# Performance work log

Measured on AMD Instinct MI355X. Metric: run time of the kernel, lower is better.

## Reference

```python
import jax, jax.numpy as jnp
import numpy as np

BEAM_SIZE = 16


def setup_inputs() -> dict:
    key = jax.random.key(0)
    ks = jax.random.split(key, 9)
    B, N, S, A, Ai, E = 4, 48, 32, 16, 8, 512
    unaries = jax.random.normal(ks[0], (B, N, S), jnp.float32)
    behaviors = jax.random.normal(ks[1], (B, N, S, A), jnp.float32)
    interactions = jax.random.normal(ks[2], (B, N, N, S, S, Ai), jnp.float32)
    masks = jnp.ones((B, N), jnp.bool_)
    behavior_masks = jax.random.bernoulli(ks[3], 0.5, (S, A))
    interaction_masks = jax.random.bernoulli(ks[4], 0.5, (S, S, Ai))
    binary_edges = jax.random.randint(ks[5], (B, E, 2), 0, N, jnp.int32)
    binary_masks = jnp.ones((B, E), jnp.bool_)
    targets = jax.random.randint(ks[6], (B, N), 0, S, jnp.int32)
    weight_param_unary = jax.random.uniform(ks[7], (S,), jnp.float32)
    weight_param_binary = jax.random.uniform(ks[8], (S, S), jnp.float32)
    return dict(unaries=unaries, behaviors=behaviors, interactions=interactions,
                weight_param_unary=weight_param_unary, weight_param_binary=weight_param_binary,
                masks=masks, behavior_masks=behavior_masks, interaction_masks=interaction_masks,
                binary_edges=binary_edges, binary_masks=binary_masks, targets=targets)


def _forward(unaries, behaviors, interactions, weight_param_unary, weight_param_binary,
             masks, behavior_masks, interaction_masks, binary_edges, binary_masks, targets):
    sg = jax.lax.stop_gradient  # mirrors torch.no_grad blocks
    B, N, S = unaries.shape
    E = binary_edges.shape[1]
    K = min(BEAM_SIZE, S)
    dt = unaries.dtype

    m = masks[..., None].astype(dt)                                  # (B,N,1)
    masked_unaries = sg(unaries * m)                                 # no_grad
    bmask = behavior_masks.astype(dt)                                # (S,A)
    acnt = bmask.sum(-1)
    acnt = jnp.where(acnt == 0, jnp.ones((), dt), acnt)              # (S,)
    behaviors_unaries = sg(((behaviors * bmask).sum(-1) / acnt) * m) # (B,N,S), no_grad

    weighted_unaries = masked_unaries + weight_param_unary * behaviors_unaries

    # --- beam selection (targets forced to beam slot 0 via +inf scatter) ---
    bi = jnp.arange(B)[:, None]
    ni = jnp.arange(N)[None, :]
    _u = weighted_unaries.at[bi, ni, targets].set(jnp.inf)
    beam_targets = jax.lax.top_k(sg(_u), K)[1]                       # (B,N,K) int
    beam_unary = jnp.take_along_axis(weighted_unaries, beam_targets, axis=2)  # (B,N,K)

    # --- binary potentials: masked mean over interaction actions ---
    imask = interaction_masks.astype(dt)                             # (S,S,Ai)
    icnt = imask.sum(-1)
    icnt = jnp.where(icnt == 0, jnp.ones((), dt), icnt)              # (S,S)
    masked_inter = (interactions * imask).sum(-1) / icnt             # (B,N,N,S,S)

    eb = jnp.arange(B)[:, None]
    sel = masked_inter[eb, binary_edges[..., 0], binary_edges[..., 1]]  # (B,E,S,S)
    bt1 = beam_targets[eb, binary_edges[..., 0]]                     # (B,E,K)
    bt2 = beam_targets[eb, binary_edges[..., 1]]                     # (B,E,K)
    bin_phis_init = sg(sel[jnp.arange(B)[:, None, None, None],
                           jnp.arange(E)[None, :, None, None],
                           bt1[:, :, :, None], bt2[:, :, None, :]])  # (B,E,K,K), no_grad
    bin_phis = bin_phis_init * weight_param_binary[bt1[:, :, :, None], bt2[:, :, None, :]]

    # --- piecewise pseudo-likelihood loss ---
    norm_unary = jax.nn.log_softmax(beam_unary, axis=-1)
    gold_unary = jnp.where(masks, norm_unary[:, :, 0], jnp.zeros((), dt))
    pll = gold_unary.sum(-1)                                         # (B,)
    norm_bin = jax.nn.log_softmax(bin_phis.reshape(B, E, K * K), axis=-1).reshape(B, E, K, K)
    gold_bin = jnp.where(binary_masks, norm_bin[:, :, 0, 0], jnp.zeros((), dt))
    pll = pll + gold_bin.sum(-1)
    nll = -(pll / masks.sum(-1).astype(dt)).mean()
    return nll


def reference(unaries, behaviors, interactions, weight_param_unary, weight_param_binary,
              masks, behavior_masks, interaction_masks, binary_edges, binary_masks, targets):
    return _forward(unaries, behaviors, interactions, weight_param_unary, weight_param_binary,
                    masks, behavior_masks, interaction_masks, binary_edges, binary_masks, targets)
```

## Files before the change

kernel.cpp:

```cpp
#include <hip/hip_runtime.h>
#include <hip/hip_bf16.h>
#include <math.h>

#define BB 4
#define NN 48
#define SS 32
#define AA 16
#define AI 8
#define EE 512
#define KK 16
#define NNODE (BB * NN)
#define NEDGE (BB * EE)

#define WS_CBIN  0
#define WS_BEAM  32768
#define WS_NG    45056
#define WS_EG    46080

__device__ __forceinline__ bool read_mask(const void* p, int idx, int flag) {
    if (flag == 1) return ((const unsigned char*)p)[idx] != 0;
    if (flag == 2) return ((const float*)p)[idx] != 0.0f;
    return ((const int*)p)[idx] != 0;
}

__device__ __forceinline__ int detect_flag(const void* bmask, int lane) {
    unsigned int wrd = ((const unsigned int*)bmask)[lane & 31];
    bool anyF = __any(wrd == 0x3F800000u);
    bool anyG = __any(wrd > 1u);
    return anyF ? 2 : (anyG ? 1 : 0);
}

__global__ __launch_bounds__(256) void node_kernel(
    const float* __restrict__ unaries,
    const float* __restrict__ behaviors,
    const float* __restrict__ wpu,
    const float* __restrict__ wpb,
    const void* masks, const void* bmask, const void* imask,
    const int* __restrict__ targets,
    float* __restrict__ cbin,
    int* __restrict__ beam,
    float* __restrict__ node_gold)
{
    int tid = threadIdx.x;
    int wid = tid >> 6, lane = tid & 63;
    int flag = detect_flag(bmask, lane);

    if (blockIdx.x < 48) {
        int node = blockIdx.x * 4 + wid;
        float m = read_mask(masks, node, flag) ? 1.f : 0.f;
        int tgt = targets[node];

        float val = -INFINITY, key = -INFINITY;
        if (lane < SS) {
            int s = lane;
            float u = unaries[node * SS + s];
            const float* bp = behaviors + ((size_t)node * SS + s) * AA;
            float cnt = 0.f, raw = 0.f;
            #pragma unroll
            for (int a = 0; a < AA; ++a) {
                bool mm = read_mask(bmask, s * AA + a, flag);
                cnt += mm ? 1.f : 0.f;
                raw += mm ? bp[a] : 0.f;
            }
            if (cnt == 0.f) cnt = 1.f;
            val = m * (u + wpu[s] * (raw / cnt));
            key = (s == tgt) ? INFINITY : val;
        }

        int rank = 0;
        #pragma unroll
        for (int t = 0; t < SS; ++t) {
            float kt = __shfl(key, t, 64);
            rank += (kt > key) || (kt == key && t < lane);
        }
        bool sel = (lane < SS) && (rank < KK);
        if (sel) beam[node * KK + rank] = lane;

        float mv = sel ? val : -INFINITY;
        #pragma unroll
        for (int off = 32; off >= 1; off >>= 1)
            mv = fmaxf(mv, __shfl_xor(mv, off, 64));
        float se = sel ? expf(val - mv) : 0.f;
        #pragma unroll
        for (int off = 32; off >= 1; off >>= 1)
            se += __shfl_xor(se, off, 64);
        float vt = __shfl(val, tgt, 64);
        if (lane == 0)
            node_gold[node] = (m > 0.f) ? (vt - mv - logf(se)) : 0.f;
    } else {
        int idx = (blockIdx.x - 48) * 256 + tid;
        int p = idx >> 3;
        float cnt = 0.f;
        #pragma unroll
        for (int a = 0; a < AI; ++a)
            cnt += read_mask(imask, p * AI + a, flag) ? 1.f : 0.f;
        if (cnt == 0.f) cnt = 1.f;
        bool mm = read_mask(imask, idx, flag);
        cbin[idx] = mm ? (wpb[p] / cnt) : 0.f;
    }
}

__global__ __launch_bounds__(256) void edge_kernel(
    const float* __restrict__ interactions,
    const int* __restrict__ edges,
    const void* binmask, const void* bmask,
    const float* __restrict__ cbin,
    const int* __restrict__ beam,
    float* __restrict__ edge_gold)
{
    int be = blockIdx.x;
    int b = be >> 9;
    int tid = threadIdx.x;
    int wid = tid >> 6, lane = tid & 63;

    int n1 = edges[be * 2 + 0];
    int n2 = edges[be * 2 + 1];

    int i = tid >> 4, j = tid & 15;
    int s1 = beam[(b * NN + n1) * KK + i];
    int s2 = beam[(b * NN + n2) * KK + j];
    int p = s1 * SS + s2;

    size_t base = (((size_t)(b * NN + n1) * NN + n2) * (SS * SS) + p) * AI;
    float4 x0 = *(const float4*)(interactions + base);
    float4 x1 = *(const float4*)(interactions + base + 4);
    float4 c0 = *(const float4*)(cbin + p * AI);
    float4 c1 = *(const float4*)(cbin + p * AI + 4);
    float phi = x0.x * c0.x + x0.y * c0.y + x0.z * c0.z + x0.w * c0.w
              + x1.x * c1.x + x1.y * c1.y + x1.z * c1.z + x1.w * c1.w;

    __shared__ float sred[4];
    float v = phi;
    #pragma unroll
    for (int off = 32; off >= 1; off >>= 1)
        v = fmaxf(v, __shfl_xor(v, off, 64));
    if (lane == 0) sred[wid] = v;
    __syncthreads();
    float mx = fmaxf(fmaxf(sred[0], sred[1]), fmaxf(sred[2], sred[3]));
    __syncthreads();
    float e = expf(phi - mx);
    #pragma unroll
    for (int off = 32; off >= 1; off >>= 1)
        e += __shfl_xor(e, off, 64);
    if (lane == 0) sred[wid] = e;
    __syncthreads();
    if (tid == 0) {
        int flag = detect_flag(bmask, lane);
        float s = sred[0] + sred[1] + sred[2] + sred[3];
        float gold = phi - mx - logf(s);
        bool bm = read_mask(binmask, be, flag);
        edge_gold[be] = bm ? gold : 0.f;
    }
}

__global__ __launch_bounds__(256) void final_kernel(
    const void* masks, const void* bmask,
    const float* __restrict__ node_gold,
    const float* __restrict__ edge_gold,
    float* __restrict__ out)
{
    int tid = threadIdx.x;
    int b = tid >> 6;
    int lane = tid & 63;
    int flag = detect_flag(bmask, lane);

    float sum = 0.f, cnt = 0.f;
    if (lane < NN) {
        sum += node_gold[b * NN + lane];
        cnt += read_mask(masks, b * NN + lane, flag) ? 1.f : 0.f;
    }
    for (int e = lane; e < EE; e += 64)
        sum += edge_gold[b * EE + e];

    #pragma unroll
    for (int off = 32; off >= 1; off >>= 1) {
        sum += __shfl_xor(sum, off, 64);
        cnt += __shfl_xor(cnt, off, 64);
    }
    __shared__ float sp[4];
    if (lane == 0) sp[b] = sum / cnt;
    __syncthreads();
    if (tid == 0)
        out[0] = -(sp[0] + sp[1] + sp[2] + sp[3]) * (1.f / BB);
}

extern "C" void kernel_launch(void* const* d_in, const int* in_sizes, int n_in,
                              void* d_out, int out_size, void* d_ws, size_t ws_size,
                              hipStream_t stream) {
    const float* unaries      = (const float*)d_in[0];
    const float* behaviors    = (const float*)d_in[1];
    const float* interactions = (const float*)d_in[2];
    const float* wpu          = (const float*)d_in[3];
    const float* wpb          = (const float*)d_in[4];
    const void*  masks        = d_in[5];
    const void*  bmask        = d_in[6];
    const void*  imask        = d_in[7];
    const int*   edges        = (const int*)d_in[8];
    const void*  binmask      = d_in[9];
    const int*   targets      = (const int*)d_in[10];
    float* out = (float*)d_out;

    char* ws = (char*)d_ws;
    float* cbin      = (float*)(ws + WS_CBIN);
    int*   beamp     = (int*)(ws + WS_BEAM);
    float* node_gold = (float*)(ws + WS_NG);
    float* edge_gold = (float*)(ws + WS_EG);

    node_kernel<<<80, 256, 0, stream>>>(unaries, behaviors, wpu, wpb,
                                        masks, bmask, imask, targets,
                                        cbin, beamp, node_gold);
    edge_kernel<<<NEDGE, 256, 0, stream>>>(interactions, edges, binmask, bmask,
                                           cbin, beamp, edge_gold);
    final_kernel<<<1, 256, 0, stream>>>(masks, bmask, node_gold, edge_gold, out);
}
```

Before: 21.64 us.

## Fuse node beam selection into edge kernel, recomputing beams per edge

Merges the node and edge kernels into a single launch. Each 64-thread edge block recomputes the beam for both endpoint nodes in its two half-waves, so the beam and the precomputed binary coefficients no longer pass through global workspace and one launch plus its dependency disappear. Each lane now handles four pairs and computes the masked interaction average inline, and the block-level reductions become single-wave shuffles with no LDS barriers. The cost is redundant unary and behavior recomputation for every edge, plus mask reads repeated per pair.

```diff
diff --git a/kernel.cpp b/kernel.cpp
--- a/kernel.cpp
+++ b/kernel.cpp
@@ -12,10 +12,8 @@
 #define NNODE (BB * NN)
 #define NEDGE (BB * EE)
 
-#define WS_CBIN  0
-#define WS_BEAM  32768
-#define WS_NG    45056
-#define WS_EG    46080
+#define WS_NG    0
+#define WS_EG    1024
 
 __device__ __forceinline__ bool read_mask(const void* p, int idx, int flag) {
     if (flag == 1) return ((const unsigned char*)p)[idx] != 0;
@@ -30,126 +28,133 @@
     return anyF ? 2 : (anyG ? 1 : 0);
 }
 
-__global__ __launch_bounds__(256) void node_kernel(
+__device__ __forceinline__ void node_vals(
+    int node, int s, int half, int flag,
+    const float* __restrict__ unaries, const float* __restrict__ behaviors,
+    const void* masks, const int* __restrict__ targets,
+    const float* __restrict__ wpu, const void* bmask,
+    float& val, int& rank, float& m, int& tgt)
+{
+    m = read_mask(masks, node, flag) ? 1.f : 0.f;
+    tgt = targets[node];
+
+    float u = unaries[node * SS + s];
+    const float* bp = behaviors + ((size_t)node * SS + s) * AA;
+    float cnt = 0.f, raw = 0.f;
+    #pragma unroll
+    for (int a = 0; a < AA; ++a) {
+        bool mm = read_mask(bmask, s * AA + a, flag);
+        cnt += mm ? 1.f : 0.f;
+        raw += mm ? bp[a] : 0.f;
+    }
+    if (cnt == 0.f) cnt = 1.f;
+    val = m * (u + wpu[s] * (raw / cnt));
+    float key = (s == tgt) ? INFINITY : val;
+
+    rank = 0;
+    int base = half << 5;
+    #pragma unroll
+    for (int t = 0; t < SS; ++t) {
+        float kt = __shfl(key, base + t, 64);
+        rank += (kt > key) || (kt == key && t < s);
+    }
+}
+
+__global__ __launch_bounds__(64) void fusedA(
     const float* __restrict__ unaries,
     const float* __restrict__ behaviors,
+    const float* __restrict__ interactions,
     const float* __restrict__ wpu,
     const float* __restrict__ wpb,
     const void* masks, const void* bmask, const void* imask,
+    const int* __restrict__ edges, const void* binmask,
     const int* __restrict__ targets,
-    float* __restrict__ cbin,
-    int* __restrict__ beam,
-    float* __restrict__ node_gold)
+    float* __restrict__ node_gold,
+    float* __restrict__ edge_gold)
 {
-    int tid = threadIdx.x;
-    int wid = tid >> 6, lane = tid & 63;
+    int lane = threadIdx.x;
+    int half = lane >> 5;
+    int s = lane & 31;
     int flag = detect_flag(bmask, lane);
 
-    if (blockIdx.x < 48) {
-        int node = blockIdx.x * 4 + wid;
-        float m = read_mask(masks, node, flag) ? 1.f : 0.f;
-        int tgt = targets[node];
-
-        float val = -INFINITY, key = -INFINITY;
-        if (lane < SS) {
-            int s = lane;
-            float u = unaries[node * SS + s];
-            const float* bp = behaviors + ((size_t)node * SS + s) * AA;
+    if (blockIdx.x < NEDGE) {
+        int be = blockIdx.x;
+        int b = be >> 9;
+        int n1 = edges[be * 2 + 0];
+        int n2 = edges[be * 2 + 1];
+        int nodeA = b * NN + n1, nodeB = b * NN + n2;
+        int node = half ? nodeB : nodeA;
+
+        __shared__ int beamLDS[2 * KK];
+        float val, m; int rank, tgt;
+        node_vals(node, s, half, flag, unaries, behaviors, masks, targets,
+                  wpu, bmask, val, rank, m, tgt);
+        if (rank < KK) beamLDS[(half << 4) + rank] = s;
+        __syncthreads();
+
+        size_t slice = (((size_t)nodeA * NN) + n2) * (SS * SS * AI);
+        float phis[4];
+        int pp[4];
+        #pragma unroll
+        for (int q = 0; q < 4; ++q) {
+            int pidx = (lane << 2) + q;
+            int i = pidx >> 4, j = pidx & 15;
+            pp[q] = beamLDS[i] * SS + beamLDS[16 + j];
+        }
+        float4 xv[4][2];
+        #pragma unroll
+        for (int q = 0; q < 4; ++q) {
+            const float* xp = interactions + slice + (size_t)pp[q] * AI;
+            xv[q][0] = *(const float4*)(xp);
+            xv[q][1] = *(const float4*)(xp + 4);
+        }
+        #pragma unroll
+        for (int q = 0; q < 4; ++q) {
+            int p = pp[q];
             float cnt = 0.f, raw = 0.f;
+            const float* x = (const float*)&xv[q][0];
             #pragma unroll
-            for (int a = 0; a < AA; ++a) {
-                bool mm = read_mask(bmask, s * AA + a, flag);
+            for (int a = 0; a < AI; ++a) {
+                bool mm = read_mask(imask, p * AI + a, flag);
                 cnt += mm ? 1.f : 0.f;
-                raw += mm ? bp[a] : 0.f;
+                raw += mm ? x[a] : 0.f;
             }
             if (cnt == 0.f) cnt = 1.f;
-            val = m * (u + wpu[s] * (raw / cnt));
-            key = (s == tgt) ? INFINITY : val;
-        }
-
-        int rank = 0;
-        #pragma unroll
-        for (int t = 0; t < SS; ++t) {
-            float kt = __shfl(key, t, 64);
-            rank += (kt > key) || (kt == key && t < lane);
-        }
-        bool sel = (lane < SS) && (rank < KK);
-        if (sel) beam[node * KK + rank] = lane;
+            phis[q] = wpb[p] * (raw / cnt);
+        }
+
+        float mx = fmaxf(fmaxf(phis[0], phis[1]), fmaxf(phis[2], phis[3]));
+        #pragma unroll
+        for (int off = 32; off >= 1; off >>= 1)
+            mx = fmaxf(mx, __shfl_xor(mx, off, 64));
+        float e = expf(phis[0] - mx) + expf(phis[1] - mx)
+                + expf(phis[2] - mx) + expf(phis[3] - mx);
+        #pragma unroll
+        for (int off = 32; off >= 1; off >>= 1)
+            e += __shfl_xor(e, off, 64);
+        if (lane == 0) {
+            float gold = phis[0] - mx - logf(e);
+            bool bm = read_mask(binmask, be, flag);
+            edge_gold[be] = bm ? gold : 0.f;
+        }
+    } else {
+        int node = blockIdx.x - NEDGE;
+        float val, m; int rank, tgt;
+        node_vals(node, s, half, flag, unaries, behaviors, masks, targets,
+                  wpu, bmask, val, rank, m, tgt);
+        bool sel = rank < KK;
 
         float mv = sel ? val : -INFINITY;
         #pragma unroll
-        for (int off = 32; off >= 1; off >>= 1)
+        for (int off = 16; off >= 1; off >>= 1)
             mv = fmaxf(mv, __shfl_xor(mv, off, 64));
         float se = sel ? expf(val - mv) : 0.f;
         #pragma unroll
-        for (int off = 32; off >= 1; off >>= 1)
+        for (int off = 16; off >= 1; off >>= 1)
             se += __shfl_xor(se, off, 64);
         float vt = __shfl(val, tgt, 64);
         if (lane == 0)
             node_gold[node] = (m > 0.f) ? (vt - mv - logf(se)) : 0.f;
-    } else {
-        int idx = (blockIdx.x - 48) * 256 + tid;
-        int p = idx >> 3;
-        float cnt = 0.f;
-        #pragma unroll
-        for (int a = 0; a < AI; ++a)
-            cnt += read_mask(imask, p * AI + a, flag) ? 1.f : 0.f;
-        if (cnt == 0.f) cnt = 1.f;
-        bool mm = read_mask(imask, idx, flag);
-        cbin[idx] = mm ? (wpb[p] / cnt) : 0.f;
-    }
-}
-
-__global__ __launch_bounds__(256) void edge_kernel(
-    const float* __restrict__ interactions,
-    const int* __restrict__ edges,
-    const void* binmask, const void* bmask,
-    const float* __restrict__ cbin,
-    const int* __restrict__ beam,
-    float* __restrict__ edge_gold)
-{
-    int be = blockIdx.x;
-    int b = be >> 9;
-    int tid = threadIdx.x;
-    int wid = tid >> 6, lane = tid & 63;
-
-    int n1 = edges[be * 2 + 0];
-    int n2 = edges[be * 2 + 1];
-
-    int i = tid >> 4, j = tid & 15;
-    int s1 = beam[(b * NN + n1) * KK + i];
-    int s2 = beam[(b * NN + n2) * KK + j];
-    int p = s1 * SS + s2;
-
-    size_t base = (((size_t)(b * NN + n1) * NN + n2) * (SS * SS) + p) * AI;
-    float4 x0 = *(const float4*)(interactions + base);
-    float4 x1 = *(const float4*)(interactions + base + 4);
-    float4 c0 = *(const float4*)(cbin + p * AI);
-    float4 c1 = *(const float4*)(cbin + p * AI + 4);
-    float phi = x0.x * c0.x + x0.y * c0.y + x0.z * c0.z + x0.w * c0.w
-              + x1.x * c1.x + x1.y * c1.y + x1.z * c1.z + x1.w * c1.w;
-
-    __shared__ float sred[4];
-    float v = phi;
-    #pragma unroll
-    for (int off = 32; off >= 1; off >>= 1)
-        v = fmaxf(v, __shfl_xor(v, off, 64));
-    if (lane == 0) sred[wid] = v;
-    __syncthreads();
-    float mx = fmaxf(fmaxf(sred[0], sred[1]), fmaxf(sred[2], sred[3]));
-    __syncthreads();
-    float e = expf(phi - mx);
-    #pragma unroll
-    for (int off = 32; off >= 1; off >>= 1)
-        e += __shfl_xor(e, off, 64);
-    if (lane == 0) sred[wid] = e;
-    __syncthreads();
-    if (tid == 0) {
-        int flag = detect_flag(bmask, lane);
-        float s = sred[0] + sred[1] + sred[2] + sred[3];
-        float gold = phi - mx - logf(s);
-        bool bm = read_mask(binmask, be, flag);
-        edge_gold[be] = bm ? gold : 0.f;
     }
 }
 
@@ -201,15 +206,12 @@
     float* out = (float*)d_out;
 
     char* ws = (char*)d_ws;
-    float* cbin      = (float*)(ws + WS_CBIN);
-    int*   beamp     = (int*)(ws + WS_BEAM);
     float* node_gold = (float*)(ws + WS_NG);
     float* edge_gold = (float*)(ws + WS_EG);
 
-    node_kernel<<<80, 256, 0, stream>>>(unaries, behaviors, wpu, wpb,
-                                        masks, bmask, imask, targets,
-                                        cbin, beamp, node_gold);
-    edge_kernel<<<NEDGE, 256, 0, stream>>>(interactions, edges, binmask, bmask,
-                                           cbin, beamp, edge_gold);
+    fusedA<<<NEDGE + NNODE, 64, 0, stream>>>(unaries, behaviors, interactions,
+                                             wpu, wpb, masks, bmask, imask,
+                                             edges, binmask, targets,
+                                             node_gold, edge_gold);
     final_kernel<<<1, 256, 0, stream>>>(masks, bmask, node_gold, edge_gold, out);
 }
```

Measured after the change: 30.13 us. +39.3%, slower.

## Assign one wavefront per edge with four beam pairs per lane

Applied to the files above, without the earlier changes.

The edge kernel now gives each 64-lane wavefront one edge instead of one 256-thread block per edge. Each lane handles four of the 256 beam pairs, and the beam indices are loaded once and spread with shuffles. This removes the shared-memory reductions and the block-wide __syncthreads, and cuts the grid from 2048 blocks to 512. More loads are in flight per lane, which costs extra registers.

```diff
diff --git a/kernel.cpp b/kernel.cpp
--- a/kernel.cpp
+++ b/kernel.cpp
@@ -108,46 +108,58 @@
     const int* __restrict__ beam,
     float* __restrict__ edge_gold)
 {
-    int be = blockIdx.x;
-    int b = be >> 9;
     int tid = threadIdx.x;
     int wid = tid >> 6, lane = tid & 63;
+    int be = (blockIdx.x << 2) + wid;
+    int b = be >> 9;
 
     int n1 = edges[be * 2 + 0];
     int n2 = edges[be * 2 + 1];
 
-    int i = tid >> 4, j = tid & 15;
-    int s1 = beam[(b * NN + n1) * KK + i];
-    int s2 = beam[(b * NN + n2) * KK + j];
-    int p = s1 * SS + s2;
-
-    size_t base = (((size_t)(b * NN + n1) * NN + n2) * (SS * SS) + p) * AI;
-    float4 x0 = *(const float4*)(interactions + base);
-    float4 x1 = *(const float4*)(interactions + base + 4);
-    float4 c0 = *(const float4*)(cbin + p * AI);
-    float4 c1 = *(const float4*)(cbin + p * AI + 4);
-    float phi = x0.x * c0.x + x0.y * c0.y + x0.z * c0.z + x0.w * c0.w
-              + x1.x * c1.x + x1.y * c1.y + x1.z * c1.z + x1.w * c1.w;
-
-    __shared__ float sred[4];
-    float v = phi;
+    int bv = 0;
+    if (lane < 32) {
+        int node = (lane < 16) ? (b * NN + n1) : (b * NN + n2);
+        bv = beam[node * KK + (lane & 15)];
+    }
+
+    size_t slice = (((size_t)(b * NN + n1) * NN) + n2) * (SS * SS * AI);
+    int pp[4];
+    float4 xv[4][2], cv[4][2];
+    #pragma unroll
+    for (int q = 0; q < 4; ++q) {
+        int pidx = (lane << 2) + q;
+        int s1 = __shfl(bv, pidx >> 4, 64);
+        int s2 = __shfl(bv, 16 + (pidx & 15), 64);
+        int p = s1 * SS + s2;
+        pp[q] = p;
+        const float* xp = interactions + slice + (size_t)p * AI;
+        xv[q][0] = *(const float4*)(xp);
+        xv[q][1] = *(const float4*)(xp + 4);
+        cv[q][0] = *(const float4*)(cbin + p * AI);
+        cv[q][1] = *(const float4*)(cbin + p * AI + 4);
+    }
+
+    float phis[4];
+    #pragma unroll
+    for (int q = 0; q < 4; ++q) {
+        float4 x0 = xv[q][0], x1 = xv[q][1];
+        float4 c0 = cv[q][0], c1 = cv[q][1];
+        phis[q] = x0.x * c0.x + x0.y * c0.y + x0.z * c0.z + x0.w * c0.w
+                + x1.x * c1.x + x1.y * c1.y + x1.z * c1.z + x1.w * c1.w;
+    }
+
+    float mx = fmaxf(fmaxf(phis[0], phis[1]), fmaxf(phis[2], phis[3]));
     #pragma unroll
     for (int off = 32; off >= 1; off >>= 1)
-        v = fmaxf(v, __shfl_xor(v, off, 64));
-    if (lane == 0) sred[wid] = v;
-    __syncthreads();
-    float mx = fmaxf(fmaxf(sred[0], sred[1]), fmaxf(sred[2], sred[3]));
-    __syncthreads();
-    float e = expf(phi - mx);
+        mx = fmaxf(mx, __shfl_xor(mx, off, 64));
+    float e = expf(phis[0] - mx) + expf(phis[1] - mx)
+            + expf(phis[2] - mx) + expf(phis[3] - mx);
     #pragma unroll
     for (int off = 32; off >= 1; off >>= 1)
         e += __shfl_xor(e, off, 64);
-    if (lane == 0) sred[wid] = e;
-    __syncthreads();
-    if (tid == 0) {
+    if (lane == 0) {
         int flag = detect_flag(bmask, lane);
-        float s = sred[0] + sred[1] + sred[2] + sred[3];
-        float gold = phi - mx - logf(s);
+        float gold = phis[0] - mx - logf(e);
         bool bm = read_mask(binmask, be, flag);
         edge_gold[be] = bm ? gold : 0.f;
     }
@@ -209,7 +221,7 @@
     node_kernel<<<80, 256, 0, stream>>>(unaries, behaviors, wpu, wpb,
                                         masks, bmask, imask, targets,
                                         cbin, beamp, node_gold);
-    edge_kernel<<<NEDGE, 256, 0, stream>>>(interactions, edges, binmask, bmask,
-                                           cbin, beamp, edge_gold);
+    edge_kernel<<<512, 256, 0, stream>>>(interactions, edges, binmask, bmask,
+                                         cbin, beamp, edge_gold);
     final_kernel<<<1, 256, 0, stream>>>(masks, bmask, node_gold, edge_gold, out);
 }
```

Result: slower. 24.19 us (+11.8%).

## Fuse final reduction into edge kernel via atomics and last-block pattern

Applied to the files above, without the earlier changes.

Drops the separate final_kernel launch. Each edge block atomically adds its gold term into a per-batch accumulator and bumps a global counter, and the last block to finish computes the loss. Removing one launch and its serialization gap is the main saving. In exchange there are 2048 contended atomics on four addresses and on one counter, and the sum now depends on the order of the float atomic adds.

```diff
diff --git a/kernel.cpp b/kernel.cpp
--- a/kernel.cpp
+++ b/kernel.cpp
@@ -15,7 +15,8 @@
 #define WS_CBIN  0
 #define WS_BEAM  32768
 #define WS_NG    45056
-#define WS_EG    46080
+#define WS_ACC   46080
+#define WS_CNT   46208
 
 __device__ __forceinline__ bool read_mask(const void* p, int idx, int flag) {
     if (flag == 1) return ((const unsigned char*)p)[idx] != 0;
@@ -39,7 +40,9 @@
     const int* __restrict__ targets,
     float* __restrict__ cbin,
     int* __restrict__ beam,
-    float* __restrict__ node_gold)
+    float* __restrict__ node_gold,
+    float* __restrict__ accE,
+    int* __restrict__ counter)
 {
     int tid = threadIdx.x;
     int wid = tid >> 6, lane = tid & 63;
@@ -88,6 +91,10 @@
         if (lane == 0)
             node_gold[node] = (m > 0.f) ? (vt - mv - logf(se)) : 0.f;
     } else {
+        if (blockIdx.x == 48 && tid < 5) {
+            if (tid < 4) accE[tid] = 0.f;
+            else *counter = 0;
+        }
         int idx = (blockIdx.x - 48) * 256 + tid;
         int p = idx >> 3;
         float cnt = 0.f;
@@ -103,10 +110,13 @@
 __global__ __launch_bounds__(256) void edge_kernel(
     const float* __restrict__ interactions,
     const int* __restrict__ edges,
-    const void* binmask, const void* bmask,
+    const void* binmask, const void* bmask, const void* masks,
     const float* __restrict__ cbin,
     const int* __restrict__ beam,
-    float* __restrict__ edge_gold)
+    const float* __restrict__ node_gold,
+    float* __restrict__ accE,
+    int* __restrict__ counter,
+    float* __restrict__ out)
 {
     int be = blockIdx.x;
     int b = be >> 9;
@@ -130,6 +140,7 @@
               + x1.x * c1.x + x1.y * c1.y + x1.z * c1.z + x1.w * c1.w;
 
     __shared__ float sred[4];
+    __shared__ int s_last;
     float v = phi;
     #pragma unroll
     for (int off = 32; off >= 1; off >>= 1)
@@ -149,39 +160,35 @@
         float s = sred[0] + sred[1] + sred[2] + sred[3];
         float gold = phi - mx - logf(s);
         bool bm = read_mask(binmask, be, flag);
-        edge_gold[be] = bm ? gold : 0.f;
+        atomicAdd(&accE[b], bm ? gold : 0.f);
+        asm volatile("s_waitcnt vmcnt(0)" ::: "memory");
+        int prev = atomicAdd(counter, 1);
+        s_last = (prev == NEDGE - 1) ? 1 : 0;
     }
-}
-
-__global__ __launch_bounds__(256) void final_kernel(
-    const void* masks, const void* bmask,
-    const float* __restrict__ node_gold,
-    const float* __restrict__ edge_gold,
-    float* __restrict__ out)
-{
-    int tid = threadIdx.x;
-    int b = tid >> 6;
-    int lane = tid & 63;
-    int flag = detect_flag(bmask, lane);
-
-    float sum = 0.f, cnt = 0.f;
-    if (lane < NN) {
-        sum += node_gold[b * NN + lane];
-        cnt += read_mask(masks, b * NN + lane, flag) ? 1.f : 0.f;
+    __syncthreads();
+
+    if (s_last) {
+        int bb = wid;
+        int flag = detect_flag(bmask, lane);
+        float sum = 0.f, cnt = 0.f;
+        if (lane < NN) {
+            sum = node_gold[bb * NN + lane];
+            cnt = read_mask(masks, bb * NN + lane, flag) ? 1.f : 0.f;
+        }
+        #pragma unroll
+        for (int off = 32; off >= 1; off >>= 1) {
+            sum += __shfl_xor(sum, off, 64);
+            cnt += __shfl_xor(cnt, off, 64);
+        }
+        __syncthreads();
+        if (lane == 0) {
+            float etot = atomicAdd(&accE[bb], 0.f);
+            sred[bb] = (sum + etot) / cnt;
+        }
+        __syncthreads();
+        if (tid == 0)
+            out[0] = -(sred[0] + sred[1] + sred[2] + sred[3]) * (1.f / BB);
     }
-    for (int e = lane; e < EE; e += 64)
-        sum += edge_gold[b * EE + e];
-
-    #pragma unroll
-    for (int off = 32; off >= 1; off >>= 1) {
-        sum += __shfl_xor(sum, off, 64);
-        cnt += __shfl_xor(cnt, off, 64);
-    }
-    __shared__ float sp[4];
-    if (lane == 0) sp[b] = sum / cnt;
-    __syncthreads();
-    if (tid == 0)
-        out[0] = -(sp[0] + sp[1] + sp[2] + sp[3]) * (1.f / BB);
 }
 
 extern "C" void kernel_launch(void* const* d_in, const int* in_sizes, int n_in,
@@ -204,12 +211,13 @@
     float* cbin      = (float*)(ws + WS_CBIN);
     int*   beamp     = (int*)(ws + WS_BEAM);
     float* node_gold = (float*)(ws + WS_NG);
-    float* edge_gold = (float*)(ws + WS_EG);
+    float* accE      = (float*)(ws + WS_ACC);
+    int*   counter   = (int*)(ws + WS_CNT);
 
     node_kernel<<<80, 256, 0, stream>>>(unaries, behaviors, wpu, wpb,
                                         masks, bmask, imask, targets,
-                                        cbin, beamp, node_gold);
+                                        cbin, beamp, node_gold, accE, counter);
     edge_kernel<<<NEDGE, 256, 0, stream>>>(interactions, edges, binmask, bmask,
-                                           cbin, beamp, edge_gold);
-    final_kernel<<<1, 256, 0, stream>>>(masks, bmask, node_gold, edge_gold, out);
-}
+                                           masks, cbin, beamp, node_gold,
+                                           accE, counter, out);
+}
```

Measured after the change: 49.47 us. 2.29x slower.
